# Optimization experiments

Measured on AMD Instinct MI355X. Metric: run time of the kernel, lower is better.

Reference implementation:

```python
import jax, jax.numpy as jnp
import numpy as np

N = 8192
NUM_CLASSES = 81            # background + 80 fg classes (COCO)
SCORE_THRESH = 0.05
NMS_THRESH = 0.5
NUM_DETECTIONS = 100
REG_W = (10.0, 10.0, 5.0, 5.0)
MIN_SIZE = 1.0
BBOX_XFORM_CLIP = float(np.log(1000.0 / 16.0))


def setup_inputs() -> dict:
    key = jax.random.key(0)
    k1, k2, k3, k4 = jax.random.split(key, 4)
    xy1 = jax.random.uniform(k1, (N, 2), minval=0.0, maxval=700.0)
    wh = jax.random.uniform(k2, (N, 2), minval=8.0, maxval=300.0)
    proposal = jnp.concatenate([xy1, xy1 + wh], axis=1)          # [N,4] xyxy
    class_logit = jax.random.normal(k3, (N, NUM_CLASSES), dtype=jnp.float32)
    box_regression = jax.random.normal(k4, (N, NUM_CLASSES * 4), dtype=jnp.float32) * 0.5
    return {"proposal": proposal, "class_logit": class_logit,
            "box_regression": box_regression, "image_h": 800, "image_w": 1216}


def _decode(deltas, boxes):
    # deltas [..., N, 4] (per-class), boxes [N, 4] xyxy; standard Fast R-CNN BoxCoder.decode
    wx, wy, ww, wh = REG_W
    widths = boxes[:, 2] - boxes[:, 0]
    heights = boxes[:, 3] - boxes[:, 1]
    cx = boxes[:, 0] + 0.5 * widths
    cy = boxes[:, 1] + 0.5 * heights
    dx = deltas[..., 0] / wx
    dy = deltas[..., 1] / wy
    dw = jnp.minimum(deltas[..., 2] / ww, BBOX_XFORM_CLIP)
    dh = jnp.minimum(deltas[..., 3] / wh, BBOX_XFORM_CLIP)
    pcx = dx * widths + cx
    pcy = dy * heights + cy
    pw = jnp.exp(dw) * widths
    ph = jnp.exp(dh) * heights
    return jnp.stack([pcx - 0.5 * pw, pcy - 0.5 * ph,
                      pcx + 0.5 * pw, pcy + 0.5 * ph], axis=-1)


def _iou_one(box, boxes):
    # IoU of one box [4] against all boxes [N,4]
    lt = jnp.maximum(box[:2], boxes[:, :2])
    rb = jnp.minimum(box[2:], boxes[:, 2:])
    whc = jnp.clip(rb - lt, 0.0)
    inter = whc[:, 0] * whc[:, 1]
    a1 = (box[2] - box[0]) * (box[3] - box[1])
    a2 = (boxes[:, 2] - boxes[:, 0]) * (boxes[:, 3] - boxes[:, 1])
    return inter / (a1 + a2 - inter + 1e-12)


def _nms_per_class(boxes, scores):
    # Sequential greedy NMS: pick highest score, suppress IoU>thresh, repeat.
    # boxes [N,4], scores [N] (already 0 where filtered). Returns top NUM_DETECTIONS.
    def step(scores_w, _):
        j = jnp.argmax(scores_w)
        s = scores_w[j]
        valid = s > 0.0
        bj = boxes[j]
        iou = _iou_one(bj, boxes)                         # [N]
        new = jnp.where(iou > NMS_THRESH, 0.0, scores_w).at[j].set(0.0)
        new = jnp.where(valid, new, scores_w)
        return new, (bj, s, valid)
    _, (sel_b, sel_s, sel_v) = jax.lax.scan(step, scores, None, length=NUM_DETECTIONS)
    return sel_b, sel_s, sel_v                            # [D,4], [D], [D]


def reference(proposal, class_logit, box_regression, image_h, image_w):
    pred_score = jax.nn.softmax(class_logit, axis=-1)     # [N, C]
    deltas = box_regression.reshape(N, NUM_CLASSES, 4)
    fg_deltas = jnp.transpose(deltas[:, 1:, :], (1, 0, 2))  # [C-1, N, 4]
    boxes = _decode(fg_deltas, proposal)                    # [C-1, N, 4]
    # clip to image (process_box)
    W = jnp.float32(image_w); H = jnp.float32(image_h)
    x1 = jnp.clip(boxes[..., 0], 0.0, W)
    y1 = jnp.clip(boxes[..., 1], 0.0, H)
    x2 = jnp.clip(boxes[..., 2], 0.0, W)
    y2 = jnp.clip(boxes[..., 3], 0.0, H)
    boxes = jnp.stack([x1, y1, x2, y2], axis=-1)            # [C-1, N, 4]
    keep_size = ((x2 - x1) >= MIN_SIZE) & ((y2 - y1) >= MIN_SIZE)
    scores = jnp.transpose(pred_score[:, 1:])               # [C-1, N]
    scores = jnp.where((scores >= SCORE_THRESH) & keep_size, scores, 0.0)
    sel_b, sel_s, sel_v = jax.vmap(_nms_per_class)(boxes, scores)  # [C-1,D,...]
    out_boxes = sel_b.reshape(-1, 4)                         # [(C-1)*D, 4]
    out_scores = sel_s.reshape(-1)
    out_labels = jnp.repeat(jnp.arange(1, NUM_CLASSES, dtype=jnp.int32), NUM_DETECTIONS)
    out_valid = sel_v.reshape(-1)
    return out_boxes, out_scores, out_labels, out_valid
```

## Files before the change

### kernel.cpp

```cpp
#include <hip/hip_runtime.h>
#include <hip/hip_bf16.h>

#define NN 8192
#define NC 81
#define FG 80
#define ND 100
#define SH 8
#define CAPS 128
#define CPADI 32
#define MAXK 384
#define BBOX_CLIP 4.135166556742356f

__global__ __launch_bounds__(256) void decode_kernel(
    const float* __restrict__ prop,
    const float* __restrict__ logit,
    const float* __restrict__ reg,
    const int* __restrict__ ih, const int* __restrict__ iw,
    int* __restrict__ counts,
    float* __restrict__ boxes0,
    float* __restrict__ cbox,
    float* __restrict__ cscore)
{
    const int n = blockIdx.x * 4 + (threadIdx.x >> 6);
    const int shard = blockIdx.x & (SH - 1);
    const int lane = threadIdx.x & 63;
    const float* lrow = logit + (long)n * NC;

    float v1 = lrow[lane];
    float v2 = (lane < NC - 64) ? lrow[64 + lane] : -1e30f;
    float m = fmaxf(v1, v2);
#pragma unroll
    for (int off = 32; off; off >>= 1) m = fmaxf(m, __shfl_xor(m, off));
    float e = expf(v1 - m) + ((lane < NC - 64) ? expf(v2 - m) : 0.0f);
#pragma unroll
    for (int off = 32; off; off >>= 1) e += __shfl_xor(e, off);

    const float W = (float)iw[0];
    const float H = (float)ih[0];
    const float4 p = *(const float4*)(prop + n * 4);
    const float pw = p.z - p.x, ph = p.w - p.y;
    const float pcx = p.x + 0.5f * pw, pcy = p.y + 0.5f * ph;

    for (int c = 1 + lane; c <= FG; c += 64) {
        float score = expf(lrow[c] - m) / e;
        const float4 d = *(const float4*)(reg + (long)n * (NC * 4) + c * 4);
        float dx = d.x / 10.0f;
        float dy = d.y / 10.0f;
        float dw = fminf(d.z / 5.0f, BBOX_CLIP);
        float dh = fminf(d.w / 5.0f, BBOX_CLIP);
        float ncx = dx * pw + pcx;
        float ncy = dy * ph + pcy;
        float nw = expf(dw) * pw;
        float nh = expf(dh) * ph;
        float bx1 = ncx - 0.5f * nw, by1 = ncy - 0.5f * nh;
        float bx2 = ncx + 0.5f * nw, by2 = ncy + 0.5f * nh;
        bx1 = fminf(fmaxf(bx1, 0.0f), W);
        by1 = fminf(fmaxf(by1, 0.0f), H);
        bx2 = fminf(fmaxf(bx2, 0.0f), W);
        by2 = fminf(fmaxf(by2, 0.0f), H);
        bool keep = ((bx2 - bx1) >= 1.0f) && ((by2 - by1) >= 1.0f);

        if (n == 0) {
            float* b0 = boxes0 + (c - 1) * 4;
            b0[0] = bx1; b0[1] = by1; b0[2] = bx2; b0[3] = by2;
        }
        if (score >= 0.05f && keep) {
            const int slot = (c - 1) * SH + shard;
            int pos = atomicAdd(&counts[slot * CPADI], 1);
            if (pos < CAPS) {
                float* cb = cbox + ((long)slot * CAPS + pos) * 4;
                cb[0] = bx1; cb[1] = by1; cb[2] = bx2; cb[3] = by2;
                cscore[slot * CAPS + pos] = score;
            }
        }
    }
}

__global__ __launch_bounds__(256) void nms_kernel(
    const int* __restrict__ counts,
    const float* __restrict__ boxes0,
    const float* __restrict__ cbox,
    const float* __restrict__ cscore,
    float* __restrict__ out)
{
    __shared__ __align__(16) float s_sc[MAXK];
    __shared__ float4 s_ubox[MAXK];
    __shared__ int    s_sidx[MAXK];
    __shared__ float4 s_box[MAXK];
    __shared__ float  s_ss[MAXK];
    __shared__ int    s_off[SH + 1];

    const int c = blockIdx.x;
    const int t = threadIdx.x;
    const int lane = t & 63;
    const int wv = t >> 6;

    if (t == 0) {
        int acc = 0;
        for (int s = 0; s < SH; ++s) {
            s_off[s] = acc;
            acc += min(counts[(c * SH + s) * CPADI], CAPS);
        }
        s_off[SH] = acc;
    }
    __syncthreads();
    const int K = min(s_off[SH], MAXK);

    for (int i = K + t; i < MAXK; i += 256) s_sc[i] = 0.0f;

    for (int sl = t; sl < SH * CAPS; sl += 256) {
        const int s = sl >> 7;
        const int i = sl & (CAPS - 1);
        const int cnt = s_off[s + 1] - s_off[s];
        if (i < cnt) {
            const int d = s_off[s] + i;
            if (d < MAXK) {
                const long src = (long)(c * SH + s) * CAPS + i;
                s_sc[d] = cscore[src];
                s_ubox[d] = *(const float4*)(cbox + src * 4);
            }
        }
    }
    __syncthreads();

    for (int i = t; i < K; i += 256) {
        const float si = s_sc[i];
        const float4* s4 = (const float4*)s_sc;
        const int nch = (K + 3) >> 2;
        int r = 0;
        for (int ch = 0; ch < nch; ++ch) {
            const float4 sj = s4[ch];
            const int j = ch * 4;
            r += (sj.x > si) || (sj.x == si && (j + 0) < i);
            r += (sj.y > si) || (sj.y == si && (j + 1) < i);
            r += (sj.z > si) || (sj.z == si && (j + 2) < i);
            r += (sj.w > si) || (sj.w == si && (j + 3) < i);
        }
        s_sidx[r] = i;
    }
    __syncthreads();

    for (int r = t; r < K; r += 256) {
        const int i = s_sidx[r];
        s_box[r] = s_ubox[i];
        s_ss[r] = s_sc[i];
    }
    __syncthreads();

    if (wv != 0) return;

    float* ob = out + (long)c * ND * 4;
    float* os = out + (long)FG * ND * 4 + c * ND;
    float* ol = os + FG * ND;
    float* ov = ol + FG * ND;
    const float lab = (float)(c + 1);

    float4 KB0 = make_float4(0.f, 0.f, 0.f, 0.f);
    float4 KB1 = make_float4(0.f, 0.f, 0.f, 0.f);
    float KA0 = 0.0f, KA1 = 0.0f;

    int kept = 0;
    float4 nb = (K > 0) ? s_box[0] : make_float4(0.f, 0.f, 0.f, 0.f);
    for (int i = 0; i < K; ++i) {
        if (kept >= ND) break;
        const float4 cb = nb;
        nb = s_box[(i + 1 < K) ? i + 1 : i];
        const float ca = (cb.z - cb.x) * (cb.w - cb.y);

        bool sup;
        {
            const float lx = fmaxf(cb.x, KB0.x), ly = fmaxf(cb.y, KB0.y);
            const float rx = fminf(cb.z, KB0.z), ry = fminf(cb.w, KB0.w);
            const float w = fmaxf(rx - lx, 0.0f), h = fmaxf(ry - ly, 0.0f);
            const float inter = w * h;
            const float iou = inter / (ca + KA0 - inter + 1e-12f);
            sup = (lane < kept) && (iou > 0.5f);
        }
        if (kept > 64) {
            const float lx = fmaxf(cb.x, KB1.x), ly = fmaxf(cb.y, KB1.y);
            const float rx = fminf(cb.z, KB1.z), ry = fminf(cb.w, KB1.w);
            const float w = fmaxf(rx - lx, 0.0f), h = fmaxf(ry - ly, 0.0f);
            const float inter = w * h;
            const float iou = inter / (ca + KA1 - inter + 1e-12f);
            sup = sup || ((lane + 64 < kept) && (iou > 0.5f));
        }
        if (__ballot(sup) == 0ull) {
            if (kept < 64) {
                if (lane == kept) { KB0 = cb; KA0 = ca; }
            } else {
                if (lane == kept - 64) { KB1 = cb; KA1 = ca; }
            }
            if (lane == 0) {
                ob[kept * 4 + 0] = cb.x; ob[kept * 4 + 1] = cb.y;
                ob[kept * 4 + 2] = cb.z; ob[kept * 4 + 3] = cb.w;
                os[kept] = s_ss[i]; ol[kept] = lab; ov[kept] = 1.0f;
            }
            ++kept;
        }
    }

    const float b0x1 = boxes0[c * 4 + 0], b0y1 = boxes0[c * 4 + 1];
    const float b0x2 = boxes0[c * 4 + 2], b0y2 = boxes0[c * 4 + 3];
    for (int d = kept + lane; d < ND; d += 64) {
        ob[d * 4 + 0] = b0x1; ob[d * 4 + 1] = b0y1;
        ob[d * 4 + 2] = b0x2; ob[d * 4 + 3] = b0y2;
        os[d] = 0.0f; ol[d] = lab; ov[d] = 0.0f;
    }
}

extern "C" void kernel_launch(void* const* d_in, const int* in_sizes, int n_in,
                              void* d_out, int out_size, void* d_ws, size_t ws_size,
                              hipStream_t stream) {
    const float* prop  = (const float*)d_in[0];
    const float* logit = (const float*)d_in[1];
    const float* reg   = (const float*)d_in[2];
    const int*   ih    = (const int*)d_in[3];
    const int*   iw    = (const int*)d_in[4];
    float* out = (float*)d_out;

    char* ws = (char*)d_ws;
    int*   counts = (int*)ws;
    float* boxes0 = (float*)(ws + 81920);
    float* cscore = (float*)(ws + 90112);
    float* cbox   = (float*)(ws + 90112 + (size_t)FG * SH * CAPS * 4);

    hipMemsetAsync(counts, 0, FG * SH * CPADI * sizeof(int), stream);
    decode_kernel<<<NN / 4, 256, 0, stream>>>(prop, logit, reg, ih, iw,
                                              counts, boxes0, cbox, cscore);
    nms_kernel<<<FG, 256, 0, stream>>>(counts, boxes0, cbox, cscore, out);
}
```

Measured before the change: 128.1 us.

## Split NMS into sort and register-resident greedy suppression scan kernels

Splits the NMS kernel into a sort kernel that writes per-class sorted scores and boxes to workspace, and a single-wave scan kernel. The scan holds all candidates in registers (six per lane), picks the next survivor with a ballot and count-trailing-zeros, and suppresses by zeroing scores. The loop now runs once per kept box rather than once per candidate. In exchange it adds a kernel launch and a global-memory round trip for the sorted data.

```diff
diff --git a/kernel.cpp b/kernel.cpp
--- a/kernel.cpp
+++ b/kernel.cpp
@@ -76,24 +76,20 @@
     }
 }
 
-__global__ __launch_bounds__(256) void nms_kernel(
+__global__ __launch_bounds__(256) void sort_kernel(
     const int* __restrict__ counts,
-    const float* __restrict__ boxes0,
     const float* __restrict__ cbox,
     const float* __restrict__ cscore,
-    float* __restrict__ out)
+    float* __restrict__ ssc,
+    float* __restrict__ sbx)
 {
     __shared__ __align__(16) float s_sc[MAXK];
     __shared__ float4 s_ubox[MAXK];
     __shared__ int    s_sidx[MAXK];
-    __shared__ float4 s_box[MAXK];
-    __shared__ float  s_ss[MAXK];
     __shared__ int    s_off[SH + 1];
 
     const int c = blockIdx.x;
     const int t = threadIdx.x;
-    const int lane = t & 63;
-    const int wv = t >> 6;
 
     if (t == 0) {
         int acc = 0;
@@ -140,14 +136,39 @@
     }
     __syncthreads();
 
-    for (int r = t; r < K; r += 256) {
-        const int i = s_sidx[r];
-        s_box[r] = s_ubox[i];
-        s_ss[r] = s_sc[i];
-    }
-    __syncthreads();
-
-    if (wv != 0) return;
+    for (int r = t; r < MAXK; r += 256) {
+        if (r < K) {
+            const int i = s_sidx[r];
+            ssc[(long)c * MAXK + r] = s_sc[i];
+            *(float4*)(sbx + ((long)c * MAXK + r) * 4) = s_ubox[i];
+        } else {
+            ssc[(long)c * MAXK + r] = 0.0f;
+            *(float4*)(sbx + ((long)c * MAXK + r) * 4) =
+                make_float4(0.f, 0.f, 0.f, 0.f);
+        }
+    }
+}
+
+__global__ __launch_bounds__(64) void scan_kernel(
+    const float* __restrict__ ssc,
+    const float* __restrict__ sbx,
+    const float* __restrict__ boxes0,
+    float* __restrict__ out)
+{
+    const int c = blockIdx.x;
+    const int lane = threadIdx.x;
+
+    float4 B0, B1, B2, B3, B4, B5;
+    float  S0, S1, S2, S3, S4, S5;
+    float  A0, A1, A2, A3, A4, A5;
+#define LOADS(s, B, S, A) {                                                  \
+        const long idx = (long)c * MAXK + (s) * 64 + lane;                   \
+        B = *(const float4*)(sbx + idx * 4);                                 \
+        S = ssc[idx];                                                        \
+        A = (B.z - B.x) * (B.w - B.y); }
+    LOADS(0, B0, S0, A0) LOADS(1, B1, S1, A1) LOADS(2, B2, S2, A2)
+    LOADS(3, B3, S3, A3) LOADS(4, B4, S4, A4) LOADS(5, B5, S5, A5)
+#undef LOADS
 
     float* ob = out + (long)c * ND * 4;
     float* os = out + (long)FG * ND * 4 + c * ND;
@@ -155,48 +176,55 @@
     float* ov = ol + FG * ND;
     const float lab = (float)(c + 1);
 
-    float4 KB0 = make_float4(0.f, 0.f, 0.f, 0.f);
-    float4 KB1 = make_float4(0.f, 0.f, 0.f, 0.f);
-    float KA0 = 0.0f, KA1 = 0.0f;
-
     int kept = 0;
-    float4 nb = (K > 0) ? s_box[0] : make_float4(0.f, 0.f, 0.f, 0.f);
-    for (int i = 0; i < K; ++i) {
-        if (kept >= ND) break;
-        const float4 cb = nb;
-        nb = s_box[(i + 1 < K) ? i + 1 : i];
-        const float ca = (cb.z - cb.x) * (cb.w - cb.y);
-
-        bool sup;
-        {
-            const float lx = fmaxf(cb.x, KB0.x), ly = fmaxf(cb.y, KB0.y);
-            const float rx = fminf(cb.z, KB0.z), ry = fminf(cb.w, KB0.w);
-            const float w = fmaxf(rx - lx, 0.0f), h = fmaxf(ry - ly, 0.0f);
-            const float inter = w * h;
-            const float iou = inter / (ca + KA0 - inter + 1e-12f);
-            sup = (lane < kept) && (iou > 0.5f);
-        }
-        if (kept > 64) {
-            const float lx = fmaxf(cb.x, KB1.x), ly = fmaxf(cb.y, KB1.y);
-            const float rx = fminf(cb.z, KB1.z), ry = fminf(cb.w, KB1.w);
-            const float w = fmaxf(rx - lx, 0.0f), h = fmaxf(ry - ly, 0.0f);
-            const float inter = w * h;
-            const float iou = inter / (ca + KA1 - inter + 1e-12f);
-            sup = sup || ((lane + 64 < kept) && (iou > 0.5f));
-        }
-        if (__ballot(sup) == 0ull) {
-            if (kept < 64) {
-                if (lane == kept) { KB0 = cb; KA0 = ca; }
-            } else {
-                if (lane == kept - 64) { KB1 = cb; KA1 = ca; }
-            }
-            if (lane == 0) {
-                ob[kept * 4 + 0] = cb.x; ob[kept * 4 + 1] = cb.y;
-                ob[kept * 4 + 2] = cb.z; ob[kept * 4 + 3] = cb.w;
-                os[kept] = s_ss[i]; ol[kept] = lab; ov[kept] = 1.0f;
-            }
-            ++kept;
-        }
+    while (kept < ND) {
+        const unsigned long long m0 = __ballot(S0 > 0.0f);
+        const unsigned long long m1 = __ballot(S1 > 0.0f);
+        const unsigned long long m2 = __ballot(S2 > 0.0f);
+        const unsigned long long m3 = __ballot(S3 > 0.0f);
+        const unsigned long long m4 = __ballot(S4 > 0.0f);
+        const unsigned long long m5 = __ballot(S5 > 0.0f);
+
+        int slot, owner;
+        if      (m0) { slot = 0; owner = __builtin_ctzll(m0); }
+        else if (m1) { slot = 1; owner = __builtin_ctzll(m1); }
+        else if (m2) { slot = 2; owner = __builtin_ctzll(m2); }
+        else if (m3) { slot = 3; owner = __builtin_ctzll(m3); }
+        else if (m4) { slot = 4; owner = __builtin_ctzll(m4); }
+        else if (m5) { slot = 5; owner = __builtin_ctzll(m5); }
+        else break;
+
+        float4 kb; float ksc;
+        if      (slot == 0) { kb = B0; ksc = S0; }
+        else if (slot == 1) { kb = B1; ksc = S1; }
+        else if (slot == 2) { kb = B2; ksc = S2; }
+        else if (slot == 3) { kb = B3; ksc = S3; }
+        else if (slot == 4) { kb = B4; ksc = S4; }
+        else                { kb = B5; ksc = S5; }
+        kb.x = __shfl(kb.x, owner);
+        kb.y = __shfl(kb.y, owner);
+        kb.z = __shfl(kb.z, owner);
+        kb.w = __shfl(kb.w, owner);
+        ksc  = __shfl(ksc, owner);
+        const float ka = (kb.z - kb.x) * (kb.w - kb.y);
+
+        if (lane == 0) {
+            ob[kept * 4 + 0] = kb.x; ob[kept * 4 + 1] = kb.y;
+            ob[kept * 4 + 2] = kb.z; ob[kept * 4 + 3] = kb.w;
+            os[kept] = ksc; ol[kept] = lab; ov[kept] = 1.0f;
+        }
+        ++kept;
+
+#define SUP(B, S, A) {                                                       \
+        const float lx = fmaxf(kb.x, B.x), ly = fmaxf(kb.y, B.y);            \
+        const float rx = fminf(kb.z, B.z), ry = fminf(kb.w, B.w);            \
+        const float w = fmaxf(rx - lx, 0.0f), h = fmaxf(ry - ly, 0.0f);      \
+        const float inter = w * h;                                           \
+        const float iou = inter / (ka + A - inter + 1e-12f);                 \
+        if (iou > 0.5f) S = 0.0f; }
+        SUP(B0, S0, A0) SUP(B1, S1, A1) SUP(B2, S2, A2)
+        SUP(B3, S3, A3) SUP(B4, S4, A4) SUP(B5, S5, A5)
+#undef SUP
     }
 
     const float b0x1 = boxes0[c * 4 + 0], b0y1 = boxes0[c * 4 + 1];
@@ -222,10 +250,13 @@
     int*   counts = (int*)ws;
     float* boxes0 = (float*)(ws + 81920);
     float* cscore = (float*)(ws + 90112);
-    float* cbox   = (float*)(ws + 90112 + (size_t)FG * SH * CAPS * 4);
+    float* cbox   = (float*)(ws + 90112 + 327680);
+    float* ssc    = (float*)(ws + 1728512);
+    float* sbx    = (float*)(ws + 1851392);
 
     hipMemsetAsync(counts, 0, FG * SH * CPADI * sizeof(int), stream);
     decode_kernel<<<NN / 4, 256, 0, stream>>>(prop, logit, reg, ih, iw,
                                               counts, boxes0, cbox, cscore);
-    nms_kernel<<<FG, 256, 0, stream>>>(counts, boxes0, cbox, cscore, out);
-}
+    sort_kernel<<<FG, 256, 0, stream>>>(counts, cbox, cscore, ssc, sbx);
+    scan_kernel<<<FG, 64, 0, stream>>>(ssc, sbx, boxes0, out);
+}
```

Result: slower. 147.5 us (+15.1%).

## Precompute IoU suppression bitmask matrix in parallel, then greedy scan over bitmasks

Applied to the files above, without the earlier changes.

Replaces the sequential per-candidate IoU test against kept boxes with a parallel pass in which 8 waves compute a KxK suppression bitmask into shared memory. A single wave then runs greedy NMS by repeatedly taking the lowest unsuppressed index and clearing the bits that row suppresses. The NMS block grows to 512 threads. This removes the long serial IoU and ballot chain, but adds O(K^2) IoU work and about 18KB of extra shared memory, which may lower occupancy.

```diff
diff --git a/kernel.cpp b/kernel.cpp
--- a/kernel.cpp
+++ b/kernel.cpp
@@ -9,7 +9,14 @@
 #define CAPS 128
 #define CPADI 32
 #define MAXK 384
+#define RS 6
 #define BBOX_CLIP 4.135166556742356f
+
+__device__ __forceinline__ unsigned long long rfl64(unsigned long long v) {
+    const unsigned lo = __builtin_amdgcn_readfirstlane((unsigned)v);
+    const unsigned hi = __builtin_amdgcn_readfirstlane((unsigned)(v >> 32));
+    return ((unsigned long long)hi << 32) | lo;
+}
 
 __global__ __launch_bounds__(256) void decode_kernel(
     const float* __restrict__ prop,
@@ -76,7 +83,7 @@
     }
 }
 
-__global__ __launch_bounds__(256) void nms_kernel(
+__global__ __launch_bounds__(512) void nms_kernel(
     const int* __restrict__ counts,
     const float* __restrict__ boxes0,
     const float* __restrict__ cbox,
@@ -88,6 +95,7 @@
     __shared__ int    s_sidx[MAXK];
     __shared__ float4 s_box[MAXK];
     __shared__ float  s_ss[MAXK];
+    __shared__ __align__(16) unsigned long long s_row[MAXK * RS];
     __shared__ int    s_off[SH + 1];
 
     const int c = blockIdx.x;
@@ -106,9 +114,13 @@
     __syncthreads();
     const int K = min(s_off[SH], MAXK);
 
-    for (int i = K + t; i < MAXK; i += 256) s_sc[i] = 0.0f;
-
-    for (int sl = t; sl < SH * CAPS; sl += 256) {
+    for (int i = K + t; i < MAXK; i += 512) {
+        s_sc[i] = 0.0f;
+        s_ss[i] = 0.0f;
+        s_box[i] = make_float4(0.f, 0.f, 0.f, 0.f);
+    }
+
+    for (int sl = t; sl < SH * CAPS; sl += 512) {
         const int s = sl >> 7;
         const int i = sl & (CAPS - 1);
         const int cnt = s_off[s + 1] - s_off[s];
@@ -123,7 +135,7 @@
     }
     __syncthreads();
 
-    for (int i = t; i < K; i += 256) {
+    for (int i = t; i < K; i += 512) {
         const float si = s_sc[i];
         const float4* s4 = (const float4*)s_sc;
         const int nch = (K + 3) >> 2;
@@ -140,10 +152,34 @@
     }
     __syncthreads();
 
-    for (int r = t; r < K; r += 256) {
+    for (int r = t; r < K; r += 512) {
         const int i = s_sidx[r];
         s_box[r] = s_ubox[i];
         s_ss[r] = s_sc[i];
+    }
+    __syncthreads();
+
+    float4 CB0, CB1, CB2, CB3, CB4, CB5;
+    float A0, A1, A2, A3, A4, A5;
+#define LC(Wd, CB, AA) { CB = s_box[(Wd) * 64 + lane]; AA = (CB.z - CB.x) * (CB.w - CB.y); }
+    LC(0, CB0, A0) LC(1, CB1, A1) LC(2, CB2, A2)
+    LC(3, CB3, A3) LC(4, CB4, A4) LC(5, CB5, A5)
+#undef LC
+
+    for (int r = wv; r < K; r += 8) {
+        const float4 rb = s_box[r];
+        const float ar = (rb.z - rb.x) * (rb.w - rb.y);
+#define DW(Wd, CB, AA) {                                                     \
+        const float lx = fmaxf(rb.x, CB.x), ly = fmaxf(rb.y, CB.y);          \
+        const float rx = fminf(rb.z, CB.z), ry = fminf(rb.w, CB.w);          \
+        const float w_ = fmaxf(rx - lx, 0.0f), h_ = fmaxf(ry - ly, 0.0f);    \
+        const float inter = w_ * h_;                                         \
+        const float iou = inter / (ar + AA - inter + 1e-12f);                \
+        const unsigned long long mk = __ballot(iou > 0.5f);                  \
+        if (lane == 0) s_row[r * RS + (Wd)] = mk; }
+        DW(0, CB0, A0) DW(1, CB1, A1) DW(2, CB2, A2)
+        DW(3, CB3, A3) DW(4, CB4, A4) DW(5, CB5, A5)
+#undef DW
     }
     __syncthreads();
 
@@ -155,48 +191,42 @@
     float* ov = ol + FG * ND;
     const float lab = (float)(c + 1);
 
-    float4 KB0 = make_float4(0.f, 0.f, 0.f, 0.f);
-    float4 KB1 = make_float4(0.f, 0.f, 0.f, 0.f);
-    float KA0 = 0.0f, KA1 = 0.0f;
+    const int Ku = __builtin_amdgcn_readfirstlane(K);
+    unsigned long long aw0, aw1, aw2, aw3, aw4, aw5;
+#define INIW(Wd) ((Ku >= (Wd)*64 + 64) ? ~0ull : ((Ku <= (Wd)*64) ? 0ull : ((~0ull) >> (64 - (Ku - (Wd)*64)))))
+    aw0 = INIW(0); aw1 = INIW(1); aw2 = INIW(2);
+    aw3 = INIW(3); aw4 = INIW(4); aw5 = INIW(5);
+#undef INIW
 
     int kept = 0;
-    float4 nb = (K > 0) ? s_box[0] : make_float4(0.f, 0.f, 0.f, 0.f);
-    for (int i = 0; i < K; ++i) {
-        if (kept >= ND) break;
-        const float4 cb = nb;
-        nb = s_box[(i + 1 < K) ? i + 1 : i];
-        const float ca = (cb.z - cb.x) * (cb.w - cb.y);
-
-        bool sup;
-        {
-            const float lx = fmaxf(cb.x, KB0.x), ly = fmaxf(cb.y, KB0.y);
-            const float rx = fminf(cb.z, KB0.z), ry = fminf(cb.w, KB0.w);
-            const float w = fmaxf(rx - lx, 0.0f), h = fmaxf(ry - ly, 0.0f);
-            const float inter = w * h;
-            const float iou = inter / (ca + KA0 - inter + 1e-12f);
-            sup = (lane < kept) && (iou > 0.5f);
-        }
-        if (kept > 64) {
-            const float lx = fmaxf(cb.x, KB1.x), ly = fmaxf(cb.y, KB1.y);
-            const float rx = fminf(cb.z, KB1.z), ry = fminf(cb.w, KB1.w);
-            const float w = fmaxf(rx - lx, 0.0f), h = fmaxf(ry - ly, 0.0f);
-            const float inter = w * h;
-            const float iou = inter / (ca + KA1 - inter + 1e-12f);
-            sup = sup || ((lane + 64 < kept) && (iou > 0.5f));
-        }
-        if (__ballot(sup) == 0ull) {
-            if (kept < 64) {
-                if (lane == kept) { KB0 = cb; KA0 = ca; }
-            } else {
-                if (lane == kept - 64) { KB1 = cb; KA1 = ca; }
-            }
-            if (lane == 0) {
-                ob[kept * 4 + 0] = cb.x; ob[kept * 4 + 1] = cb.y;
-                ob[kept * 4 + 2] = cb.z; ob[kept * 4 + 3] = cb.w;
-                os[kept] = s_ss[i]; ol[kept] = lab; ov[kept] = 1.0f;
-            }
-            ++kept;
-        }
+    while (kept < ND) {
+        int r;
+        if      (aw0) r = __builtin_ctzll(aw0);
+        else if (aw1) r = 64  + __builtin_ctzll(aw1);
+        else if (aw2) r = 128 + __builtin_ctzll(aw2);
+        else if (aw3) r = 192 + __builtin_ctzll(aw3);
+        else if (aw4) r = 256 + __builtin_ctzll(aw4);
+        else if (aw5) r = 320 + __builtin_ctzll(aw5);
+        else break;
+
+        const unsigned long long* rp = s_row + r * RS;
+        const unsigned long long q0 = rfl64(rp[0]);
+        const unsigned long long q1 = rfl64(rp[1]);
+        const unsigned long long q2 = rfl64(rp[2]);
+        const unsigned long long q3 = rfl64(rp[3]);
+        const unsigned long long q4 = rfl64(rp[4]);
+        const unsigned long long q5 = rfl64(rp[5]);
+
+        if (lane == 0) {
+            const float4 kb = s_box[r];
+            ob[kept * 4 + 0] = kb.x; ob[kept * 4 + 1] = kb.y;
+            ob[kept * 4 + 2] = kb.z; ob[kept * 4 + 3] = kb.w;
+            os[kept] = s_ss[r]; ol[kept] = lab; ov[kept] = 1.0f;
+        }
+        ++kept;
+
+        aw0 &= ~q0; aw1 &= ~q1; aw2 &= ~q2;
+        aw3 &= ~q3; aw4 &= ~q4; aw5 &= ~q5;
     }
 
     const float b0x1 = boxes0[c * 4 + 0], b0y1 = boxes0[c * 4 + 1];
@@ -222,10 +252,10 @@
     int*   counts = (int*)ws;
     float* boxes0 = (float*)(ws + 81920);
     float* cscore = (float*)(ws + 90112);
-    float* cbox   = (float*)(ws + 90112 + (size_t)FG * SH * CAPS * 4);
+    float* cbox   = (float*)(ws + 90112 + 327680);
 
     hipMemsetAsync(counts, 0, FG * SH * CPADI * sizeof(int), stream);
     decode_kernel<<<NN / 4, 256, 0, stream>>>(prop, logit, reg, ih, iw,
                                               counts, boxes0, cbox, cscore);
-    nms_kernel<<<FG, 256, 0, stream>>>(counts, boxes0, cbox, cscore, out);
-}
+    nms_kernel<<<FG, 512, 0, stream>>>(counts, boxes0, cbox, cscore, out);
+}
```

After: 127.4 us. About the same (-0.6%).
